# Kernel optimization log

Hardware: AMD Instinct MI355X
Metric: run time of the kernel (lower is better)

Reference implementation:

```python
import jax, jax.numpy as jnp
import numpy as np

B, N, HID, E, H = 4, 256, 256, 64, 4
OUT = HID // 2          # 128
D = OUT // H            # 32
AGG = H * (2 * D + 1)   # 260 = concat(mean D, attn_sum 1, max D) per head


def setup_inputs() -> dict:
    key = jax.random.key(0)
    ks = jax.random.split(key, 7)
    s = 0.05
    return {
        "h_x": jax.random.normal(ks[0], (B, N, HID), jnp.float32),
        "h_e": jax.random.normal(ks[1], (B, N, N, E), jnp.float32),
        "h_m": jnp.ones((B, N), jnp.float32),
        "W_Q": jax.random.normal(ks[2], (OUT, HID), jnp.float32) * s,
        "W_K": jax.random.normal(ks[3], (OUT, E), jnp.float32) * s,
        "W_V": jax.random.normal(ks[4], (OUT, E), jnp.float32) * s,
        "W_R": jax.random.normal(ks[5], (OUT, AGG), jnp.float32) * s,
    }


def reference(h_x, h_e, h_m, W_Q, W_K, W_V, W_R):
    # queries from node features: [B,H,N,D]
    h_q = (h_x @ W_Q.T).reshape(B, N, H, D).transpose(0, 2, 1, 3)
    # keys/values from dense pairwise edge features: [B,H,N,N,D]
    h_k = jnp.einsum('bnme,ce->bnmc', h_e, W_K).reshape(B, N, N, H, D).transpose(0, 3, 1, 2, 4)
    h_v = jnp.einsum('bnme,ce->bnmc', h_e, W_V).reshape(B, N, N, H, D).transpose(0, 3, 1, 2, 4)
    # broadcast dot: [B,H,N,N]
    scores = jnp.einsum('bhnd,bhnmd->bhnm', h_q, h_k) / np.float32(np.sqrt(D))
    # per-node mask broadcast as [B,1,N,1] (masks query rows)
    scores = jnp.where(h_m[:, None, :, None] == 0, -jnp.inf, scores)
    # NOTE: original code softmaxes over dim=1 = HEAD axis (faithful)
    attn = jax.nn.softmax(scores, axis=1)                      # [B,H,N,N]
    attn_w = attn[..., None] * h_v                             # [B,H,N,N,D]
    aggr_sum = attn_w.sum(axis=3)                              # [B,H,N,D]
    attn_sum = attn.sum(axis=3, keepdims=True) + 1e-8          # [B,H,N,1]
    aggr_mean = aggr_sum / attn_sum
    aggr_max = attn_w.max(axis=3)                              # [B,H,N,D]
    multi = jnp.concatenate([aggr_mean, attn_sum, aggr_max], axis=-1)  # [B,H,N,2D+1]
    aggr_out = multi.transpose(0, 2, 1, 3).reshape(B, N, AGG)  # [B,N,260]
    return aggr_out @ W_R.T                                    # [B,N,OUT]
```

## Files before the change

kernel.cpp:

```cpp
#include <hip/hip_runtime.h>

constexpr int Bb   = 4;
constexpr int Nn   = 256;
constexpr int HID  = 256;
constexpr int Ee   = 64;
constexpr int Hh   = 4;
constexpr int OUTc = 128;
constexpr int Dd   = 32;
constexpr int AGG  = 260;
constexpr int REC  = 264;
constexpr int NSL  = 4;
constexpr int QA_LD = 264;

constexpr size_t WS_WSP   = 0;
constexpr size_t WS_WRT   = WS_WSP + (size_t)Bb * Nn * NSL * REC;
constexpr size_t WS_FRAGV = WS_WRT + (size_t)AGG * OUTc;
constexpr size_t WS_FRAGQ = WS_FRAGV + 4096;
constexpr size_t WS_UFRAG = WS_FRAGQ + 16384;

typedef __attribute__((ext_vector_type(8))) short short8;
typedef __attribute__((ext_vector_type(4))) float floatx4;

__device__ __forceinline__ unsigned short f2bf(float f) {
    union { float f; unsigned u; } x; x.f = f;
    unsigned r = x.u + 0x7FFFu + ((x.u >> 16) & 1u);
    return (unsigned short)(r >> 16);
}

__device__ __forceinline__ short8 pack8(floatx4 f0, floatx4 f1) {
    short8 v;
    v[0] = (short)f2bf(f0[0]); v[1] = (short)f2bf(f0[1]);
    v[2] = (short)f2bf(f0[2]); v[3] = (short)f2bf(f0[3]);
    v[4] = (short)f2bf(f1[0]); v[5] = (short)f2bf(f1[1]);
    v[6] = (short)f2bf(f1[2]); v[7] = (short)f2bf(f1[3]);
    return v;
}

__global__ __launch_bounds__(256)
void eama_pack(const float* __restrict__ W_Q, const float* __restrict__ W_V,
               const float* __restrict__ W_R,
               unsigned short* __restrict__ wfragV, unsigned short* __restrict__ wfragQ,
               float* __restrict__ W_RT)
{
    const int tid = threadIdx.x;
    const int bid = blockIdx.x;

    if (bid < 4) {
        const int e    = bid * 256 + tid;
        const int lane = e & 63;
        const int ks   = (e >> 6) & 1;
        const int ct   = e >> 7;
        const int ncol = lane & 15, q8 = lane >> 4;
        const float* row = W_V + (ct * 16 + ncol) * Ee;
        const int k0 = ks * 32 + q8 * 8;
        floatx4 f0 = *(const floatx4*)(row + k0);
        floatx4 f1 = *(const floatx4*)(row + k0 + 4);
        *(short8*)(wfragV + (size_t)e * 8) = pack8(f0, f1);
    } else if (bid < 20) {
        const int e    = (bid - 4) * 256 + tid;
        const int lane = e & 63;
        const int ks   = (e >> 6) & 7;
        const int ct   = (e >> 9) & 1;
        const int wv   = (e >> 10) & 3;
        const int ncol = lane & 15, q8 = lane >> 4;
        const float* row = W_Q + (wv * 32 + ct * 16 + ncol) * HID;
        const int k0 = ks * 32 + q8 * 8;
        floatx4 f0 = *(const floatx4*)(row + k0);
        floatx4 f1 = *(const floatx4*)(row + k0 + 4);
        *(short8*)(wfragQ + (size_t)e * 8) = pack8(f0, f1);
    } else {
        const int i = (bid - 20) * 256 + tid;
        if (i < AGG * OUTc) {
            const int c = i & 127, j = i >> 7;
            W_RT[j * OUTc + c] = W_R[c * AGG + j];
        }
    }
}

__global__ __launch_bounds__(256)
void eama_qu(const float* __restrict__ h_x, const unsigned short* __restrict__ wfragQ,
             const float* __restrict__ W_K, unsigned short* __restrict__ ufrag)
{
    __shared__ __align__(16) unsigned short sA[16 * QA_LD];
    __shared__ __align__(16) float sqL[16][132];
    __shared__ __align__(16) float sU2[16][256];
    const int tid  = threadIdx.x;
    const int b0   = blockIdx.x * 16;
    const int lane = tid & 63;
    const int wv   = tid >> 6;
    const int ncol = lane & 15, q8 = lane >> 4;

    short8 bq[2][8];
    #pragma unroll
    for (int ct = 0; ct < 2; ++ct)
        #pragma unroll
        for (int ks = 0; ks < 8; ++ks) {
            const int e = ((wv * 2 + ct) * 8 + ks) * 64 + lane;
            bq[ct][ks] = *(const short8*)(wfragQ + (size_t)e * 8);
        }
    #pragma unroll
    for (int i = 0; i < 2; ++i) {
        const int idx = tid + i * 256;
        const int r = idx >> 5, blk = idx & 31;
        const float* src = h_x + (size_t)(b0 + r) * HID + blk * 8;
        floatx4 f0 = *(const floatx4*)(src);
        floatx4 f1 = *(const floatx4*)(src + 4);
        *(short8*)&sA[r * QA_LD + blk * 8] = pack8(f0, f1);
    }
    __syncthreads();
    floatx4 acc[2] = {(floatx4){0,0,0,0}, (floatx4){0,0,0,0}};
    #pragma unroll
    for (int ks = 0; ks < 8; ++ks) {
        short8 a = *(const short8*)&sA[ncol * QA_LD + ks * 32 + q8 * 8];
        acc[0] = __builtin_amdgcn_mfma_f32_16x16x32_bf16(a, bq[0][ks], acc[0], 0, 0, 0);
        acc[1] = __builtin_amdgcn_mfma_f32_16x16x32_bf16(a, bq[1][ks], acc[1], 0, 0, 0);
    }
    #pragma unroll
    for (int ct = 0; ct < 2; ++ct)
        #pragma unroll
        for (int rr = 0; rr < 4; ++rr)
            sqL[q8 * 4 + rr][wv * 32 + ct * 16 + ncol] = acc[ct][rr];
    __syncthreads();

    {
        const int h = wv, e = lane;
        float a16[16];
        #pragma unroll
        for (int i = 0; i < 16; ++i) a16[i] = 0.f;
        #pragma unroll
        for (int d4 = 0; d4 < 8; ++d4) {
            float wk0 = W_K[(h * Dd + d4 * 4 + 0) * Ee + e];
            float wk1 = W_K[(h * Dd + d4 * 4 + 1) * Ee + e];
            float wk2 = W_K[(h * Dd + d4 * 4 + 2) * Ee + e];
            float wk3 = W_K[(h * Dd + d4 * 4 + 3) * Ee + e];
            #pragma unroll
            for (int b16 = 0; b16 < 16; ++b16) {
                floatx4 qv = *(const floatx4*)&sqL[b16][h * Dd + d4 * 4];
                a16[b16] += (qv[0] * wk0 + qv[1] * wk1) + (qv[2] * wk2 + qv[3] * wk3);
            }
        }
        #pragma unroll
        for (int b16 = 0; b16 < 16; ++b16)
            sU2[b16][h * 64 + e] = a16[b16] * 0.1767766952966369f;
    }
    __syncthreads();

    #pragma unroll
    for (int k = 0; k < 8; ++k) {
        const int ei   = tid + k * 256;
        const int b16  = ei >> 7;
        const int rest = ei & 127;
        const int ks   = rest >> 6;
        const int l    = rest & 63;
        const int nc   = l & 15, qq = l >> 4;
        short8 v = {0, 0, 0, 0, 0, 0, 0, 0};
        if (nc < Hh) {
            floatx4 f0 = *(const floatx4*)&sU2[b16][nc * 64 + ks * 32 + qq * 8];
            floatx4 f1 = *(const floatx4*)&sU2[b16][nc * 64 + ks * 32 + qq * 8 + 4];
            v = pack8(f0, f1);
        }
        *(short8*)(ufrag + ((size_t)((b0 + b16) * 2 + ks) * 64 + l) * 8) = v;
    }
}

__global__ __launch_bounds__(256, 4)
void eama_main(const float* __restrict__ h_e, const float* __restrict__ h_m,
               const unsigned short* __restrict__ wfragV,
               const unsigned short* __restrict__ ufrag,
               float* __restrict__ wsP)
{
    __shared__ __align__(16) float sS[4][16][4];
    __shared__ float sVS[4][OUTc];
    __shared__ float sVM[4][OUTc];
    __shared__ float sAS[4][Hh];

    const int tid  = threadIdx.x;
    const int lane = tid & 63;
    const int w    = tid >> 6;
    const int ncol = lane & 15;
    const int q8   = lane >> 4;
    const int bn   = blockIdx.x;
    const int sl   = blockIdx.y;
    const float maskv = h_m[bn];

    const int m0 = sl * 64 + w * 16;
    const float* ar = h_e + ((size_t)bn * Nn + m0 + ncol) * Ee;

    floatx4 a00 = *(const floatx4*)(ar + q8 * 8);
    floatx4 a01 = *(const floatx4*)(ar + q8 * 8 + 4);
    floatx4 a10 = *(const floatx4*)(ar + 32 + q8 * 8);
    floatx4 a11 = *(const floatx4*)(ar + 32 + q8 * 8 + 4);
    short8 bu0 = *(const short8*)(ufrag + ((size_t)(bn * 2 + 0) * 64 + lane) * 8);
    short8 bu1 = *(const short8*)(ufrag + ((size_t)(bn * 2 + 1) * 64 + lane) * 8);

    short8 af0 = pack8(a00, a01);
    short8 af1 = pack8(a10, a11);

    floatx4 accV[8], accS = (floatx4){0, 0, 0, 0};
    #pragma unroll
    for (int ct = 0; ct < 8; ++ct) accV[ct] = (floatx4){0, 0, 0, 0};

    #pragma unroll
    for (int ct = 0; ct < 8; ++ct) {
        short8 bf0 = *(const short8*)(wfragV + ((size_t)(ct * 2 + 0) * 64 + lane) * 8);
        short8 bf1 = *(const short8*)(wfragV + ((size_t)(ct * 2 + 1) * 64 + lane) * 8);
        accV[ct] = __builtin_amdgcn_mfma_f32_16x16x32_bf16(af0, bf0, accV[ct], 0, 0, 0);
        accV[ct] = __builtin_amdgcn_mfma_f32_16x16x32_bf16(af1, bf1, accV[ct], 0, 0, 0);
    }
    accS = __builtin_amdgcn_mfma_f32_16x16x32_bf16(af0, bu0, accS, 0, 0, 0);
    accS = __builtin_amdgcn_mfma_f32_16x16x32_bf16(af1, bu1, accS, 0, 0, 0);

    if (ncol < Hh) {
        #pragma unroll
        for (int r = 0; r < 4; ++r)
            sS[w][q8 * 4 + r][ncol] = (maskv != 0.f) ? accS[r] : -1e30f;
    }
    __syncthreads();

    float vs[8], vm[8], asumH = 0.f;
    #pragma unroll
    for (int ct = 0; ct < 8; ++ct) { vs[ct] = 0.f; vm[ct] = -3.402823466e38f; }
    #pragma unroll
    for (int r = 0; r < 4; ++r) {
        floatx4 sc = *(const floatx4*)&sS[w][q8 * 4 + r][0];
        float mx = fmaxf(fmaxf(sc[0], sc[1]), fmaxf(sc[2], sc[3]));
        float e0 = __expf(sc[0] - mx), e1 = __expf(sc[1] - mx);
        float e2 = __expf(sc[2] - mx), e3 = __expf(sc[3] - mx);
        float inv = 1.f / ((e0 + e1) + (e2 + e3));
        float a0 = e0 * inv, a1 = e1 * inv, a2 = e2 * inv, a3 = e3 * inv;
        asumH += (ncol & 2) ? ((ncol & 1) ? a3 : a2) : ((ncol & 1) ? a1 : a0);
        float p;
        p = a0 * accV[0][r]; vs[0] += p; vm[0] = fmaxf(vm[0], p);
        p = a0 * accV[1][r]; vs[1] += p; vm[1] = fmaxf(vm[1], p);
        p = a1 * accV[2][r]; vs[2] += p; vm[2] = fmaxf(vm[2], p);
        p = a1 * accV[3][r]; vs[3] += p; vm[3] = fmaxf(vm[3], p);
        p = a2 * accV[4][r]; vs[4] += p; vm[4] = fmaxf(vm[4], p);
        p = a2 * accV[5][r]; vs[5] += p; vm[5] = fmaxf(vm[5], p);
        p = a3 * accV[6][r]; vs[6] += p; vm[6] = fmaxf(vm[6], p);
        p = a3 * accV[7][r]; vs[7] += p; vm[7] = fmaxf(vm[7], p);
    }

    #pragma unroll
    for (int ct = 0; ct < 8; ++ct) {
        vs[ct] += __shfl_xor(vs[ct], 16, 64);
        vs[ct] += __shfl_xor(vs[ct], 32, 64);
        vm[ct] = fmaxf(vm[ct], __shfl_xor(vm[ct], 16, 64));
        vm[ct] = fmaxf(vm[ct], __shfl_xor(vm[ct], 32, 64));
    }
    asumH += __shfl_xor(asumH, 16, 64);
    asumH += __shfl_xor(asumH, 32, 64);

    if (lane < 16) {
        #pragma unroll
        for (int ct = 0; ct < 8; ++ct) {
            sVS[w][ct * 16 + lane] = vs[ct];
            sVM[w][ct * 16 + lane] = vm[ct];
        }
    }
    if (lane < Hh) sAS[w][lane] = asumH;
    __syncthreads();
    if (tid < OUTc) {
        const size_t base = (size_t)(bn * NSL + sl) * REC;
        float vsum = (sVS[0][tid] + sVS[1][tid]) + (sVS[2][tid] + sVS[3][tid]);
        float vmax = fmaxf(fmaxf(sVM[0][tid], sVM[1][tid]), fmaxf(sVM[2][tid], sVM[3][tid]));
        wsP[base + tid]        = vsum;
        wsP[base + OUTc + tid] = vmax;
        if (tid < Hh)
            wsP[base + 2 * OUTc + tid] =
                (sAS[0][tid] + sAS[1][tid]) + (sAS[2][tid] + sAS[3][tid]);
    }
}

__global__ __launch_bounds__(256)
void eama_stage2(const float* __restrict__ wsP, const float* __restrict__ W_RT,
                 float* __restrict__ out)
{
    __shared__ __align__(16) float sM[REC];
    __shared__ float sAs[Hh];
    __shared__ float sAcc[2][OUTc];
    const int tid = threadIdx.x;
    const int bn  = blockIdx.x;
    const size_t base = (size_t)bn * NSL * REC;

    float vsum = 0.f, vmax = -3.402823466e38f;
    if (tid < OUTc) {
        #pragma unroll
        for (int tp = 0; tp < NSL; ++tp) {
            vsum += wsP[base + tp * REC + tid];
            vmax = fmaxf(vmax, wsP[base + tp * REC + OUTc + tid]);
        }
    }
    if (tid < Hh) {
        float a = 1e-8f;
        #pragma unroll
        for (int tp = 0; tp < NSL; ++tp) a += wsP[base + tp * REC + 2 * OUTc + tid];
        sAs[tid] = a;
    }
    __syncthreads();
    if (tid < OUTc) {
        const int h = tid >> 5, d = tid & 31;
        sM[h * 65 + d]      = vsum / sAs[h];
        sM[h * 65 + 33 + d] = vmax;
        if (tid < Hh) sM[tid * 65 + 32] = sAs[tid];
    }
    __syncthreads();
    {
        const int c = tid & 127, part = tid >> 7;
        const int j0 = part * 130;
        float acc = 0.f;
        #pragma unroll 5
        for (int j = j0; j < j0 + 130; ++j)
            acc = fmaf(sM[j], W_RT[j * OUTc + c], acc);
        sAcc[part][c] = acc;
    }
    __syncthreads();
    if (tid < OUTc)
        out[bn * OUTc + tid] = sAcc[0][tid] + sAcc[1][tid];
}

extern "C" void kernel_launch(void* const* d_in, const int* in_sizes, int n_in,
                              void* d_out, int out_size, void* d_ws, size_t ws_size,
                              hipStream_t stream) {
    const float* h_x = (const float*)d_in[0];
    const float* h_e = (const float*)d_in[1];
    const float* h_m = (const float*)d_in[2];
    const float* W_Q = (const float*)d_in[3];
    const float* W_K = (const float*)d_in[4];
    const float* W_V = (const float*)d_in[5];
    const float* W_R = (const float*)d_in[6];
    float* out = (float*)d_out;

    float* ws            = (float*)d_ws;
    float* wsP           = ws + WS_WSP;
    float* W_RT          = ws + WS_WRT;
    unsigned short* wfV  = (unsigned short*)(ws + WS_FRAGV);
    unsigned short* wfQ  = (unsigned short*)(ws + WS_FRAGQ);
    unsigned short* ufr  = (unsigned short*)(ws + WS_UFRAG);

    eama_pack<<<dim3(150), dim3(256), 0, stream>>>(W_Q, W_V, W_R, wfV, wfQ, W_RT);
    eama_qu<<<dim3(Bb * Nn / 16), dim3(256), 0, stream>>>(h_x, wfQ, W_K, ufr);
    eama_main<<<dim3(Bb * Nn, NSL), dim3(256), 0, stream>>>(h_e, h_m, wfV, ufr, wsP);
    eama_stage2<<<dim3(Bb * Nn), dim3(256), 0, stream>>>(wsP, W_RT, out);
}
```

Baseline: 135.0 us.

## Fuse main and stage2 kernels with per-block loop over all key rows

Merges the edge-attention kernel and the W_R projection stage into one kernel. Each block now handles a whole query node and loops over four 16-row tiles per wave, prefetching the next tile of h_e while computing the current one and keeping the V weight fragments in registers. This removes the partial-result workspace round trip and one kernel launch. In exchange the grid shrinks from 4096 to 1024 blocks and register pressure rises, with launch bounds relaxed to two blocks per CU.

```diff
diff --git a/kernel.cpp b/kernel.cpp
--- a/kernel.cpp
+++ b/kernel.cpp
@@ -9,11 +9,9 @@
 constexpr int Dd   = 32;
 constexpr int AGG  = 260;
 constexpr int REC  = 264;
-constexpr int NSL  = 4;
 constexpr int QA_LD = 264;
 
-constexpr size_t WS_WSP   = 0;
-constexpr size_t WS_WRT   = WS_WSP + (size_t)Bb * Nn * NSL * REC;
+constexpr size_t WS_WRT   = 0;
 constexpr size_t WS_FRAGV = WS_WRT + (size_t)AGG * OUTc;
 constexpr size_t WS_FRAGQ = WS_FRAGV + 4096;
 constexpr size_t WS_UFRAG = WS_FRAGQ + 16384;
@@ -163,16 +161,19 @@
     }
 }
 
-__global__ __launch_bounds__(256, 4)
-void eama_main(const float* __restrict__ h_e, const float* __restrict__ h_m,
+__global__ __launch_bounds__(256, 2)
+void eama_full(const float* __restrict__ h_e, const float* __restrict__ h_m,
                const unsigned short* __restrict__ wfragV,
                const unsigned short* __restrict__ ufrag,
-               float* __restrict__ wsP)
+               const float* __restrict__ W_RT, float* __restrict__ out)
 {
     __shared__ __align__(16) float sS[4][16][4];
     __shared__ float sVS[4][OUTc];
     __shared__ float sVM[4][OUTc];
     __shared__ float sAS[4][Hh];
+    __shared__ float sAsum[Hh];
+    __shared__ __align__(16) float sM[REC];
+    __shared__ float sAcc[2][OUTc];
 
     const int tid  = threadIdx.x;
     const int lane = tid & 63;
@@ -180,64 +181,84 @@
     const int ncol = lane & 15;
     const int q8   = lane >> 4;
     const int bn   = blockIdx.x;
-    const int sl   = blockIdx.y;
     const float maskv = h_m[bn];
 
-    const int m0 = sl * 64 + w * 16;
-    const float* ar = h_e + ((size_t)bn * Nn + m0 + ncol) * Ee;
-
-    floatx4 a00 = *(const floatx4*)(ar + q8 * 8);
-    floatx4 a01 = *(const floatx4*)(ar + q8 * 8 + 4);
-    floatx4 a10 = *(const floatx4*)(ar + 32 + q8 * 8);
-    floatx4 a11 = *(const floatx4*)(ar + 32 + q8 * 8 + 4);
+    short8 bfV[8][2];
+    #pragma unroll
+    for (int ct = 0; ct < 8; ++ct)
+        #pragma unroll
+        for (int ks = 0; ks < 2; ++ks)
+            bfV[ct][ks] = *(const short8*)(wfragV + ((size_t)(ct * 2 + ks) * 64 + lane) * 8);
     short8 bu0 = *(const short8*)(ufrag + ((size_t)(bn * 2 + 0) * 64 + lane) * 8);
     short8 bu1 = *(const short8*)(ufrag + ((size_t)(bn * 2 + 1) * 64 + lane) * 8);
 
-    short8 af0 = pack8(a00, a01);
-    short8 af1 = pack8(a10, a11);
-
-    floatx4 accV[8], accS = (floatx4){0, 0, 0, 0};
-    #pragma unroll
-    for (int ct = 0; ct < 8; ++ct) accV[ct] = (floatx4){0, 0, 0, 0};
-
-    #pragma unroll
-    for (int ct = 0; ct < 8; ++ct) {
-        short8 bf0 = *(const short8*)(wfragV + ((size_t)(ct * 2 + 0) * 64 + lane) * 8);
-        short8 bf1 = *(const short8*)(wfragV + ((size_t)(ct * 2 + 1) * 64 + lane) * 8);
-        accV[ct] = __builtin_amdgcn_mfma_f32_16x16x32_bf16(af0, bf0, accV[ct], 0, 0, 0);
-        accV[ct] = __builtin_amdgcn_mfma_f32_16x16x32_bf16(af1, bf1, accV[ct], 0, 0, 0);
-    }
-    accS = __builtin_amdgcn_mfma_f32_16x16x32_bf16(af0, bu0, accS, 0, 0, 0);
-    accS = __builtin_amdgcn_mfma_f32_16x16x32_bf16(af1, bu1, accS, 0, 0, 0);
-
-    if (ncol < Hh) {
-        #pragma unroll
-        for (int r = 0; r < 4; ++r)
-            sS[w][q8 * 4 + r][ncol] = (maskv != 0.f) ? accS[r] : -1e30f;
-    }
-    __syncthreads();
-
     float vs[8], vm[8], asumH = 0.f;
     #pragma unroll
     for (int ct = 0; ct < 8; ++ct) { vs[ct] = 0.f; vm[ct] = -3.402823466e38f; }
-    #pragma unroll
-    for (int r = 0; r < 4; ++r) {
-        floatx4 sc = *(const floatx4*)&sS[w][q8 * 4 + r][0];
-        float mx = fmaxf(fmaxf(sc[0], sc[1]), fmaxf(sc[2], sc[3]));
-        float e0 = __expf(sc[0] - mx), e1 = __expf(sc[1] - mx);
-        float e2 = __expf(sc[2] - mx), e3 = __expf(sc[3] - mx);
-        float inv = 1.f / ((e0 + e1) + (e2 + e3));
-        float a0 = e0 * inv, a1 = e1 * inv, a2 = e2 * inv, a3 = e3 * inv;
-        asumH += (ncol & 2) ? ((ncol & 1) ? a3 : a2) : ((ncol & 1) ? a1 : a0);
-        float p;
-        p = a0 * accV[0][r]; vs[0] += p; vm[0] = fmaxf(vm[0], p);
-        p = a0 * accV[1][r]; vs[1] += p; vm[1] = fmaxf(vm[1], p);
-        p = a1 * accV[2][r]; vs[2] += p; vm[2] = fmaxf(vm[2], p);
-        p = a1 * accV[3][r]; vs[3] += p; vm[3] = fmaxf(vm[3], p);
-        p = a2 * accV[4][r]; vs[4] += p; vm[4] = fmaxf(vm[4], p);
-        p = a2 * accV[5][r]; vs[5] += p; vm[5] = fmaxf(vm[5], p);
-        p = a3 * accV[6][r]; vs[6] += p; vm[6] = fmaxf(vm[6], p);
-        p = a3 * accV[7][r]; vs[7] += p; vm[7] = fmaxf(vm[7], p);
+
+    const float* heb = h_e + (size_t)bn * Nn * Ee;
+
+    floatx4 p0, p1, p2, p3;
+    {
+        const float* ar = heb + (size_t)(w * 64 + ncol) * Ee;
+        p0 = *(const floatx4*)(ar + q8 * 8);
+        p1 = *(const floatx4*)(ar + q8 * 8 + 4);
+        p2 = *(const floatx4*)(ar + 32 + q8 * 8);
+        p3 = *(const floatx4*)(ar + 32 + q8 * 8 + 4);
+    }
+
+    #pragma unroll
+    for (int it = 0; it < 4; ++it) {
+        floatx4 n0, n1, n2, n3;
+        if (it < 3) {
+            const float* ar = heb + (size_t)(w * 64 + (it + 1) * 16 + ncol) * Ee;
+            n0 = *(const floatx4*)(ar + q8 * 8);
+            n1 = *(const floatx4*)(ar + q8 * 8 + 4);
+            n2 = *(const floatx4*)(ar + 32 + q8 * 8);
+            n3 = *(const floatx4*)(ar + 32 + q8 * 8 + 4);
+        }
+        short8 af0 = pack8(p0, p1);
+        short8 af1 = pack8(p2, p3);
+
+        floatx4 accV[8], accS = (floatx4){0, 0, 0, 0};
+        #pragma unroll
+        for (int ct = 0; ct < 8; ++ct) accV[ct] = (floatx4){0, 0, 0, 0};
+        #pragma unroll
+        for (int ct = 0; ct < 8; ++ct) {
+            accV[ct] = __builtin_amdgcn_mfma_f32_16x16x32_bf16(af0, bfV[ct][0], accV[ct], 0, 0, 0);
+            accV[ct] = __builtin_amdgcn_mfma_f32_16x16x32_bf16(af1, bfV[ct][1], accV[ct], 0, 0, 0);
+        }
+        accS = __builtin_amdgcn_mfma_f32_16x16x32_bf16(af0, bu0, accS, 0, 0, 0);
+        accS = __builtin_amdgcn_mfma_f32_16x16x32_bf16(af1, bu1, accS, 0, 0, 0);
+
+        if (ncol < Hh) {
+            #pragma unroll
+            for (int r = 0; r < 4; ++r)
+                sS[w][q8 * 4 + r][ncol] = (maskv != 0.f) ? accS[r] : -1e30f;
+        }
+        __builtin_amdgcn_wave_barrier();
+
+        #pragma unroll
+        for (int r = 0; r < 4; ++r) {
+            floatx4 sc = *(const floatx4*)&sS[w][q8 * 4 + r][0];
+            float mx = fmaxf(fmaxf(sc[0], sc[1]), fmaxf(sc[2], sc[3]));
+            float e0 = __expf(sc[0] - mx), e1 = __expf(sc[1] - mx);
+            float e2 = __expf(sc[2] - mx), e3 = __expf(sc[3] - mx);
+            float inv = 1.f / ((e0 + e1) + (e2 + e3));
+            float a0 = e0 * inv, a1 = e1 * inv, a2 = e2 * inv, a3 = e3 * inv;
+            asumH += (ncol & 2) ? ((ncol & 1) ? a3 : a2) : ((ncol & 1) ? a1 : a0);
+            float p;
+            p = a0 * accV[0][r]; vs[0] += p; vm[0] = fmaxf(vm[0], p);
+            p = a0 * accV[1][r]; vs[1] += p; vm[1] = fmaxf(vm[1], p);
+            p = a1 * accV[2][r]; vs[2] += p; vm[2] = fmaxf(vm[2], p);
+            p = a1 * accV[3][r]; vs[3] += p; vm[3] = fmaxf(vm[3], p);
+            p = a2 * accV[4][r]; vs[4] += p; vm[4] = fmaxf(vm[4], p);
+            p = a2 * accV[5][r]; vs[5] += p; vm[5] = fmaxf(vm[5], p);
+            p = a3 * accV[6][r]; vs[6] += p; vm[6] = fmaxf(vm[6], p);
+            p = a3 * accV[7][r]; vs[7] += p; vm[7] = fmaxf(vm[7], p);
+        }
+        __builtin_amdgcn_wave_barrier();
+        p0 = n0; p1 = n1; p2 = n2; p3 = n3;
     }
 
     #pragma unroll
@@ -259,59 +280,30 @@
     }
     if (lane < Hh) sAS[w][lane] = asumH;
     __syncthreads();
+    if (tid < Hh) {
+        sAsum[tid] = 1e-8f +
+            (sAS[0][tid] + sAS[1][tid]) + (sAS[2][tid] + sAS[3][tid]);
+    }
+    __syncthreads();
     if (tid < OUTc) {
-        const size_t base = (size_t)(bn * NSL + sl) * REC;
         float vsum = (sVS[0][tid] + sVS[1][tid]) + (sVS[2][tid] + sVS[3][tid]);
         float vmax = fmaxf(fmaxf(sVM[0][tid], sVM[1][tid]), fmaxf(sVM[2][tid], sVM[3][tid]));
-        wsP[base + tid]        = vsum;
-        wsP[base + OUTc + tid] = vmax;
-        if (tid < Hh)
-            wsP[base + 2 * OUTc + tid] =
-                (sAS[0][tid] + sAS[1][tid]) + (sAS[2][tid] + sAS[3][tid]);
-    }
-}
-
-__global__ __launch_bounds__(256)
-void eama_stage2(const float* __restrict__ wsP, const float* __restrict__ W_RT,
-                 float* __restrict__ out)
-{
-    __shared__ __align__(16) float sM[REC];
-    __shared__ float sAs[Hh];
-    __shared__ float sAcc[2][OUTc];
-    const int tid = threadIdx.x;
-    const int bn  = blockIdx.x;
-    const size_t base = (size_t)bn * NSL * REC;
-
-    float vsum = 0.f, vmax = -3.402823466e38f;
-    if (tid < OUTc) {
-        #pragma unroll
-        for (int tp = 0; tp < NSL; ++tp) {
-            vsum += wsP[base + tp * REC + tid];
-            vmax = fmaxf(vmax, wsP[base + tp * REC + OUTc + tid]);
-        }
-    }
-    if (tid < Hh) {
-        float a = 1e-8f;
-        #pragma unroll
-        for (int tp = 0; tp < NSL; ++tp) a += wsP[base + tp * REC + 2 * OUTc + tid];
-        sAs[tid] = a;
-    }
-    __syncthreads();
-    if (tid < OUTc) {
         const int h = tid >> 5, d = tid & 31;
-        sM[h * 65 + d]      = vsum / sAs[h];
+        sM[h * 65 + d]      = vsum / sAsum[h];
         sM[h * 65 + 33 + d] = vmax;
-        if (tid < Hh) sM[tid * 65 + 32] = sAs[tid];
+        if (tid < Hh) sM[tid * 65 + 32] = sAsum[tid];
     }
     __syncthreads();
     {
         const int c = tid & 127, part = tid >> 7;
         const int j0 = part * 130;
-        float acc = 0.f;
+        float a0 = 0.f, a1 = 0.f;
         #pragma unroll 5
-        for (int j = j0; j < j0 + 130; ++j)
-            acc = fmaf(sM[j], W_RT[j * OUTc + c], acc);
-        sAcc[part][c] = acc;
+        for (int j = j0; j < j0 + 130; j += 2) {
+            a0 = fmaf(sM[j],     W_RT[(j)     * OUTc + c], a0);
+            a1 = fmaf(sM[j + 1], W_RT[(j + 1) * OUTc + c], a1);
+        }
+        sAcc[part][c] = a0 + a1;
     }
     __syncthreads();
     if (tid < OUTc)
@@ -331,7 +323,6 @@
     float* out = (float*)d_out;
 
     float* ws            = (float*)d_ws;
-    float* wsP           = ws + WS_WSP;
     float* W_RT          = ws + WS_WRT;
     unsigned short* wfV  = (unsigned short*)(ws + WS_FRAGV);
     unsigned short* wfQ  = (unsigned short*)(ws + WS_FRAGQ);
@@ -339,6 +330,5 @@
 
     eama_pack<<<dim3(150), dim3(256), 0, stream>>>(W_Q, W_V, W_R, wfV, wfQ, W_RT);
     eama_qu<<<dim3(Bb * Nn / 16), dim3(256), 0, stream>>>(h_x, wfQ, W_K, ufr);
-    eama_main<<<dim3(Bb * Nn, NSL), dim3(256), 0, stream>>>(h_e, h_m, wfV, ufr, wsP);
-    eama_stage2<<<dim3(Bb * Nn), dim3(256), 0, stream>>>(wsP, W_RT, out);
-}
+    eama_full<<<dim3(Bb * Nn), dim3(256), 0, stream>>>(h_e, h_m, wfV, ufr, W_RT, out);
+}
```

Measured after the change: 128.4 us. 1.05x faster.
